# Performance work log

Measured on AMD Instinct MI355X. Metric: run time of the kernel, lower is better.

Reference implementation:

```python
import jax, jax.numpy as jnp
import numpy as np

EMBED = 2048
N_EXPERTS = 64
TOP_K = 8


def setup_inputs() -> dict:
    key = jax.random.key(0)
    k_x, k_w, k_b = jax.random.split(key, 3)
    inputs = jax.random.normal(k_x, (8, 4096, EMBED), dtype=jnp.float32)
    # nn.Linear(embed_size, num_experts): weight [E, D], bias [E]
    bound = 1.0 / np.sqrt(EMBED)
    W = jax.random.uniform(k_w, (N_EXPERTS, EMBED), dtype=jnp.float32, minval=-bound, maxval=bound)
    b = jax.random.uniform(k_b, (N_EXPERTS,), dtype=jnp.float32, minval=-bound, maxval=bound)
    return {"inputs": inputs, "W": W, "b": b}


def reference(inputs, W, b):
    # scores: [B, S, E]
    scores = jnp.einsum("bsd,ed->bse", inputs, W) + b
    topk_scores, indices = jax.lax.top_k(scores, TOP_K)  # [B,S,K]
    # scatter topk_scores into a zero mask (non-selected slots stay 0.0)
    onehot = jax.nn.one_hot(indices, N_EXPERTS, dtype=scores.dtype)  # [B,S,K,E]
    mask = jnp.einsum("bske,bsk->bse", onehot, topk_scores)
    router_output = jax.nn.softmax(mask, axis=-1)
    return (router_output, indices)
```

## Files before the change

kernel.cpp:

```cpp
#include <hip/hip_runtime.h>
#include <math.h>

#define N_TOKENS 32768
#define EMBED    2048
#define NEXP     64
#define TOPK     8
#define BM       64
#define BK       64
#define NCH      (EMBED / BK)
#define SCS      65
#define THRESH   1e-4f
#define WELEMS   (NEXP * EMBED)

typedef __attribute__((ext_vector_type(8)))  short short8;
typedef __attribute__((ext_vector_type(4)))  short short4v;
typedef __attribute__((ext_vector_type(16))) float f32x16;

__device__ __forceinline__ unsigned short bf16rne(float f) {
  unsigned int fb = __float_as_uint(f);
  return (unsigned short)((fb + 0x7FFFu + ((fb >> 16) & 1u)) >> 16);
}

__device__ __forceinline__ void cvt4(float4 f, short4v* h, short4v* l) {
  float fs[4] = {f.x, f.y, f.z, f.w};
  short4v hh, ll;
#pragma unroll
  for (int i = 0; i < 4; ++i) {
    unsigned short hr = bf16rne(fs[i]);
    hh[i] = (short)hr;
    float hf = __uint_as_float((unsigned int)hr << 16);
    ll[i] = (short)bf16rne(fs[i] - hf);
  }
  *h = hh; *l = ll;
}

__global__ void split_w(const float* __restrict__ W, short* __restrict__ wh,
                        short* __restrict__ wl) {
  const int T = blockIdx.x * 256 + threadIdx.x;
  const int n = T >> 8, kg8 = T & 255;
  const float4* W4 = (const float4*)W;
  float4 a = W4[n * 512 + kg8 * 2];
  float4 b = W4[n * 512 + kg8 * 2 + 1];
  short4v h0, l0, h1, l1;
  cvt4(a, &h0, &l0); cvt4(b, &h1, &l1);
  short* dh = &wh[(kg8 * 64 + n) * 8];
  short* dl = &wl[(kg8 * 64 + n) * 8];
  *(short4v*)dh = h0; *(short4v*)(dh + 4) = h1;
  *(short4v*)dl = l0; *(short4v*)(dl + 4) = l1;
}

__global__ __launch_bounds__(256, 2)
void router_kernel(const float* __restrict__ x, const short* __restrict__ wh,
                   const short* __restrict__ wl, const float* __restrict__ bias,
                   const float* __restrict__ Wf, float* __restrict__ out) {
  __shared__ short  xs[2][2][8][64][8];
  __shared__ float  sc[BM * SCS];
  __shared__ double s_fix[NEXP];
  __shared__ int    s_list[BM];
  __shared__ int    s_cnt;

  const int tid  = threadIdx.x;
  const int t0   = blockIdx.x * BM;
  const int lane = tid & 63;
  const int w    = tid >> 6;
  const int half = lane >> 5;
  const int r5   = lane & 31;
  const int tw   = (w & 1) * 32;
  const int ew   = (w >> 1) * 32;

  if (tid == 0) s_cnt = 0;

  const int c4  = tid & 15;
  const int rr  = tid >> 4;
  const int g   = c4 >> 1;
  const int sub = c4 & 1;

  const float* xp = x + (size_t)(t0 + rr) * EMBED + (c4 << 2);
  const short8* Bh = (const short8*)wh;
  const short8* Bl = (const short8*)wl;
  const int boff = half * 64 + ew + r5;

  f32x16 acc;
#pragma unroll
  for (int i = 0; i < 16; ++i) acc[i] = 0.f;

  float4 px[4];
#pragma unroll
  for (int i = 0; i < 4; ++i)
    px[i] = *(const float4*)(xp + (size_t)(i * 16) * EMBED);

  for (int ch = 0; ch < NCH; ++ch) {
    short8 bh[4], bl[4];
#pragma unroll
    for (int s = 0; s < 4; ++s) {
      const int bi = (ch * 4 + s) * 128 + boff;
      bh[s] = Bh[bi]; bl[s] = Bl[bi];
    }
    const int buf = ch & 1;
#pragma unroll
    for (int i = 0; i < 4; ++i) {
      short4v h, l;
      cvt4(px[i], &h, &l);
      const int slot = (rr + 16 * i) ^ g;
      *(short4v*)&xs[buf][0][g][slot][sub * 4] = h;
      *(short4v*)&xs[buf][1][g][slot][sub * 4] = l;
    }
    __syncthreads();

    if (ch + 1 < NCH) {
#pragma unroll
      for (int i = 0; i < 4; ++i)
        px[i] = *(const float4*)(xp + (size_t)(i * 16) * EMBED + (ch + 1) * BK);
    }

#pragma unroll
    for (int s = 0; s < 4; ++s) {
      const int kg   = 2 * s + half;
      const int slot = (tw + r5) ^ kg;
      short8 ah = *(const short8*)&xs[buf][0][kg][slot][0];
      short8 al = *(const short8*)&xs[buf][1][kg][slot][0];
      acc = __builtin_amdgcn_mfma_f32_32x32x16_bf16(ah, bh[s], acc, 0, 0, 0);
      acc = __builtin_amdgcn_mfma_f32_32x32x16_bf16(ah, bl[s], acc, 0, 0, 0);
      acc = __builtin_amdgcn_mfma_f32_32x32x16_bf16(al, bh[s], acc, 0, 0, 0);
    }
  }

#pragma unroll
  for (int reg = 0; reg < 16; ++reg) {
    const int row = (reg & 3) + 8 * (reg >> 2) + 4 * half;
    sc[(tw + row) * SCS + ew + r5] = acc[reg];
  }
  __syncthreads();

  float* rout = out;
  float* iout = out + (size_t)N_TOKENS * NEXP;
  const float bias_l = bias[lane];

  for (int tb = 0; tb < 4; ++tb) {
    const int tbase = w * 16 + tb * 4;
    float orig[4]; unsigned cur[4];
#pragma unroll
    for (int i = 0; i < 4; ++i) {
      orig[i] = sc[(tbase + i) * SCS + lane] + bias_l;
      unsigned b = __float_as_uint(orig[i]);
      unsigned u = b ^ (((unsigned)((int)b >> 31)) | 0x80000000u);
      cur[i] = (u & 0xFFFFFFC0u) | (63u - (unsigned)lane);
    }
    float m[4], Z[4], ming[4], prev[4], morig[4];
    int myidx[4]; bool sel[4];
#pragma unroll
    for (int i = 0; i < 4; ++i) { sel[i] = false; morig[i] = 0.f; myidx[i] = 0; ming[i] = 1e30f; }

#pragma unroll
    for (int r = 0; r < 9; ++r) {
      unsigned v[4];
#pragma unroll
      for (int i = 0; i < 4; ++i) v[i] = cur[i];
#pragma unroll
      for (int s2 = 1; s2 < 64; s2 <<= 1) {
#pragma unroll
        for (int i = 0; i < 4; ++i) {
          unsigned o = (unsigned)__shfl_xor((int)v[i], s2);
          v[i] = v[i] > o ? v[i] : o;
        }
      }
#pragma unroll
      for (int i = 0; i < 4; ++i) {
        unsigned vb = (v[i] & 0x80000000u) ? (v[i] ^ 0x80000000u) : ~v[i];
        float fv = __uint_as_float(vb);
        if (r == 0) { m[i] = fmaxf(fv, 0.f); Z[i] = 56.f * expf(-m[i]) + expf(fv - m[i]); }
        else {
          ming[i] = fminf(ming[i], prev[i] - fv);
          if (r < 8) Z[i] += expf(fv - m[i]);
        }
        prev[i] = fv;
        if (r < 8) {
          if (lane == r) myidx[i] = 63 - (int)(v[i] & 63u);
          if (cur[i] == v[i]) { sel[i] = true; morig[i] = orig[i]; cur[i] = 0u; }
        }
      }
    }
#pragma unroll
    for (int i = 0; i < 4; ++i) {
      const int t = tbase + i;
      if (ming[i] < THRESH) {
        if (lane == 0) { int p = atomicAdd(&s_cnt, 1); s_list[p] = t; }
      } else {
        const float p = expf(morig[i] - m[i]) / Z[i];
        rout[(size_t)(t0 + t) * NEXP + lane] = p;
        if (lane < TOPK) iout[(size_t)(t0 + t) * TOPK + lane] = (float)myidx[i];
      }
    }
  }

  __syncthreads();
  const int cnt = s_cnt;
  const float4* x4 = (const float4*)x;
  const float4* W4 = (const float4*)Wf;

  for (int i = 0; i < cnt; ++i) {
    const int t = s_list[i];
    const int e = tid >> 2, sub2 = tid & 3;
    const float4* xr = x4 + (size_t)(t0 + t) * (EMBED / 4) + sub2 * 128;
    const float4* wr = W4 + (size_t)e * (EMBED / 4) + sub2 * 128;
    double a0 = 0.0, a1 = 0.0;
#pragma unroll 4
    for (int m4 = 0; m4 < 128; m4 += 2) {
      float4 xv = xr[m4], wv = wr[m4];
      a0 = fma((double)xv.x, (double)wv.x, a0); a0 = fma((double)xv.y, (double)wv.y, a0);
      a0 = fma((double)xv.z, (double)wv.z, a0); a0 = fma((double)xv.w, (double)wv.w, a0);
      float4 xv2 = xr[m4 + 1], wv2 = wr[m4 + 1];
      a1 = fma((double)xv2.x, (double)wv2.x, a1); a1 = fma((double)xv2.y, (double)wv2.y, a1);
      a1 = fma((double)xv2.z, (double)wv2.z, a1); a1 = fma((double)xv2.w, (double)wv2.w, a1);
    }
    double a = a0 + a1;
    a += __shfl_xor(a, 1); a += __shfl_xor(a, 2);
    if (sub2 == 0) s_fix[e] = a + (double)bias[e];
    __syncthreads();

    if (tid < 64) {
      const double orig = s_fix[lane];
      double curd = orig, vals[8];
      int myidx = 0; double mym = 0.0;
#pragma unroll
      for (int r = 0; r < 8; ++r) {
        double v = curd; int id = lane;
#pragma unroll
        for (int s2 = 1; s2 < 64; s2 <<= 1) {
          const double ov = __shfl_xor(v, s2);
          const int    oi = __shfl_xor(id, s2);
          if (ov > v || (ov == v && oi < id)) { v = ov; id = oi; }
        }
        vals[r] = v;
        if (lane == r)  myidx = id;
        if (lane == id) { mym = orig; curd = -1e300; }
      }
      const double md = fmax(vals[0], 0.0);
      double Zd = 56.0 * exp(-md);
#pragma unroll
      for (int r = 0; r < 8; ++r) Zd += exp(vals[r] - md);
      const double p = exp(mym - md) / Zd;
      rout[(size_t)(t0 + t) * NEXP + lane] = (float)p;
      if (lane < TOPK) iout[(size_t)(t0 + t) * TOPK + lane] = (float)myidx;
    }
    __syncthreads();
  }
}

extern "C" void kernel_launch(void* const* d_in, const int* in_sizes, int n_in,
                              void* d_out, int out_size, void* d_ws, size_t ws_size,
                              hipStream_t stream) {
  const float* x = (const float*)d_in[0];
  const float* W = (const float*)d_in[1];
  const float* b = (const float*)d_in[2];
  short* wh = (short*)d_ws;
  short* wl = wh + WELEMS;
  split_w<<<64, 256, 0, stream>>>(W, wh, wl);
  router_kernel<<<N_TOKENS / BM, 256, 0, stream>>>(x, wh, wl, b, W, (float*)d_out);
}
```

Before: 558.8 us.

## Stream fp32 activations directly into LDS and split to bf16 after the LDS read

Activation tiles are now copied from global memory straight into a swizzled fp32 LDS double buffer with global_load_lds, instead of passing through registers, being split into bf16 hi/lo, and written to LDS. The bf16 hi/lo split now happens per MFMA operand after each LDS read. The score scratch area aliases the LDS tile buffer, and the launch bound is raised to 4 blocks per CU to allow more overlap. The cost is that each wave repeats the split on operands it reads, and register pressure under the tighter launch bound may cause spills.

New measurement: 558.0 us. About the same (-0.2%).

```diff
diff --git a/kernel.cpp b/kernel.cpp
--- a/kernel.cpp
+++ b/kernel.cpp
@@ -49,15 +49,15 @@
   *(short4v*)dl = l0; *(short4v*)(dl + 4) = l1;
 }
 
-__global__ __launch_bounds__(256, 2)
+__global__ __launch_bounds__(256, 4)
 void router_kernel(const float* __restrict__ x, const short* __restrict__ wh,
                    const short* __restrict__ wl, const float* __restrict__ bias,
                    const float* __restrict__ Wf, float* __restrict__ out) {
-  __shared__ short  xs[2][2][8][64][8];
-  __shared__ float  sc[BM * SCS];
+  __shared__ float4 lx[2][1024];
   __shared__ double s_fix[NEXP];
   __shared__ int    s_list[BM];
   __shared__ int    s_cnt;
+  float* sc = (float*)&lx[0][0];
 
   const int tid  = threadIdx.x;
   const int t0   = blockIdx.x * BM;
@@ -70,60 +70,70 @@
 
   if (tid == 0) s_cnt = 0;
 
-  const int c4  = tid & 15;
-  const int rr  = tid >> 4;
-  const int g   = c4 >> 1;
-  const int sub = c4 & 1;
-
-  const float* xp = x + (size_t)(t0 + rr) * EMBED + (c4 << 2);
-  const short8* Bh = (const short8*)wh;
-  const short8* Bl = (const short8*)wl;
+  const float4* x4g = (const float4*)x;
+  const short8* Bh  = (const short8*)wh;
+  const short8* Bl  = (const short8*)wl;
   const int boff = half * 64 + ew + r5;
 
+  const int row16 = tid >> 4;
+  const int s4    = tid & 15;
+  const int c4sw  = s4 ^ row16;
+  const int wbase = (tid & 192);
+
   f32x16 acc;
 #pragma unroll
   for (int i = 0; i < 16; ++i) acc[i] = 0.f;
 
-  float4 px[4];
-#pragma unroll
-  for (int i = 0; i < 4; ++i)
-    px[i] = *(const float4*)(xp + (size_t)(i * 16) * EMBED);
+#pragma unroll
+  for (int i = 0; i < 4; ++i) {
+    const float4* gp = x4g + (size_t)(t0 + row16 + 16 * i) * (EMBED / 4) + c4sw;
+    __builtin_amdgcn_global_load_lds((const void*)gp, (void*)&lx[0][i * 256 + wbase],
+                                     16, 0, 0);
+  }
+
+  const int arow  = tw + r5;
+  const int am    = arow & 15;
+  const int abase = (arow >> 4) * 256 + am * 16;
 
   for (int ch = 0; ch < NCH; ++ch) {
+    const int buf = ch & 1;
+    __syncthreads();
+
+    if (ch + 1 < NCH) {
+#pragma unroll
+      for (int i = 0; i < 4; ++i) {
+        const float4* gp = x4g + (size_t)(t0 + row16 + 16 * i) * (EMBED / 4)
+                               + (ch + 1) * 16 + c4sw;
+        __builtin_amdgcn_global_load_lds((const void*)gp,
+                                         (void*)&lx[buf ^ 1][i * 256 + wbase], 16, 0, 0);
+      }
+    }
+
     short8 bh[4], bl[4];
 #pragma unroll
     for (int s = 0; s < 4; ++s) {
       const int bi = (ch * 4 + s) * 128 + boff;
       bh[s] = Bh[bi]; bl[s] = Bl[bi];
     }
-    const int buf = ch & 1;
-#pragma unroll
-    for (int i = 0; i < 4; ++i) {
-      short4v h, l;
-      cvt4(px[i], &h, &l);
-      const int slot = (rr + 16 * i) ^ g;
-      *(short4v*)&xs[buf][0][g][slot][sub * 4] = h;
-      *(short4v*)&xs[buf][1][g][slot][sub * 4] = l;
-    }
-    __syncthreads();
-
-    if (ch + 1 < NCH) {
-#pragma unroll
-      for (int i = 0; i < 4; ++i)
-        px[i] = *(const float4*)(xp + (size_t)(i * 16) * EMBED + (ch + 1) * BK);
-    }
 
 #pragma unroll
     for (int s = 0; s < 4; ++s) {
-      const int kg   = 2 * s + half;
-      const int slot = (tw + r5) ^ kg;
-      short8 ah = *(const short8*)&xs[buf][0][kg][slot][0];
-      short8 al = *(const short8*)&xs[buf][1][kg][slot][0];
+      const int c0 = s * 4 + half * 2;
+      float4 fa = lx[buf][abase + (c0 ^ am)];
+      float4 fb = lx[buf][abase + ((c0 + 1) ^ am)];
+      short4v h0, l0, h1, l1;
+      cvt4(fa, &h0, &l0); cvt4(fb, &h1, &l1);
+      short8 ah, al;
+#pragma unroll
+      for (int j = 0; j < 4; ++j) { ah[j] = h0[j]; ah[j + 4] = h1[j];
+                                    al[j] = l0[j]; al[j + 4] = l1[j]; }
       acc = __builtin_amdgcn_mfma_f32_32x32x16_bf16(ah, bh[s], acc, 0, 0, 0);
       acc = __builtin_amdgcn_mfma_f32_32x32x16_bf16(ah, bl[s], acc, 0, 0, 0);
       acc = __builtin_amdgcn_mfma_f32_32x32x16_bf16(al, bh[s], acc, 0, 0, 0);
     }
   }
+
+  __syncthreads();
 
 #pragma unroll
   for (int reg = 0; reg < 16; ++reg) {
@@ -195,13 +205,12 @@
 
   __syncthreads();
   const int cnt = s_cnt;
-  const float4* x4 = (const float4*)x;
   const float4* W4 = (const float4*)Wf;
 
   for (int i = 0; i < cnt; ++i) {
     const int t = s_list[i];
     const int e = tid >> 2, sub2 = tid & 3;
-    const float4* xr = x4 + (size_t)(t0 + t) * (EMBED / 4) + sub2 * 128;
+    const float4* xr = x4g + (size_t)(t0 + t) * (EMBED / 4) + sub2 * 128;
     const float4* wr = W4 + (size_t)e * (EMBED / 4) + sub2 * 128;
     double a0 = 0.0, a1 = 0.0;
 #pragma unroll 4
```
